# Performance work log

Measured on AMD Instinct MI355X. Metric: run time of the kernel, lower is better.

Reference implementation:

```python
import jax, jax.numpy as jnp
import numpy as np
from jax import lax

MAX_DECAY = 0.99
EPS = 1e-05
TOPK = 4


def ema_mask_group(moving_avg, new, mask, decay0, cluster_update_num):
    """Faithful port of ema_tensor_mask_group_inplace, including the quirk that
    the Python-level `decay` variable is carried (and possibly shrunk) across
    cluster iterations. Implemented as a lax.scan over clusters carrying decay.
    moving_avg/new: [C] or [C, D]; mask, cluster_update_num: [C].
    """
    def step(decay, xs):
        ma, nw, m, c = xs
        d = jnp.where((m != 0) & (c <= 10.0), decay * c / 10.0, decay)
        out = jnp.where(m != 0, ma * d + nw * (1.0 - d), ma)
        return d, out
    _, out = lax.scan(step, jnp.asarray(decay0, moving_avg.dtype),
                      (moving_avg, new, mask, cluster_update_num))
    return out


def laplace_smoothing(x, n_categories, eps=EPS):
    return (x + eps) / (x.sum() + n_categories * eps)


def setup_inputs() -> dict:
    key = jax.random.key(0)
    k1, k2 = jax.random.split(key)
    N, C, D = 65536, 512, 256
    return {
        "inputs_flatten": jax.random.normal(k1, (N, D), dtype=jnp.float32),
        "dictionary": jax.random.normal(k2, (C, D), dtype=jnp.float32),
        "cluster_size_sum": jnp.zeros((C,), dtype=jnp.float32),
        "cluster_value": jnp.zeros((C, D), dtype=jnp.float32),
        "cluster_update_num": jnp.ones((C,), dtype=jnp.float32),
    }


def reference(inputs_flatten, dictionary, cluster_size_sum, cluster_value,
              cluster_update_num):
    N, D = inputs_flatten.shape
    C = dictionary.shape[0]
    dic = lax.stop_gradient(dictionary)  # dictionary used via .detach()/.data

    # squared euclidean distances [N, C]
    distances = (jnp.sum(inputs_flatten ** 2, axis=1, keepdims=True)
                 + jnp.sum(dic ** 2, axis=1)
                 - 2.0 * jnp.matmul(inputs_flatten, dic.T))

    # ascending sort -> take topK smallest distances
    _, topk_idx = lax.top_k(-distances, TOPK)          # [N, K]
    topk_emb = dic[topk_idx]                            # [N, K, D]
    group_emb = jnp.sum(topk_emb, axis=1) / TOPK        # [N, D]

    # multi-hot encodings via scatter
    rows = jnp.arange(N)[:, None]
    encodings = jnp.zeros((N, C), dtype=jnp.float32).at[rows, topk_idx].set(1.0)

    # ---- training-mode EMA codebook update (single device: all_gather = identity) ----
    x_sg = lax.stop_gradient(inputs_flatten)
    cluster_size = jnp.sum(encodings, axis=0)           # [C]
    cluster_mask = (cluster_size != 0).astype(jnp.float32)
    cluster_update_num_new = cluster_update_num + cluster_mask

    cluster_size_sum_new = ema_mask_group(cluster_size_sum, cluster_size,
                                          cluster_mask, MAX_DECAY,
                                          cluster_update_num_new)
    input_sum = jnp.matmul(encodings.T, x_sg)           # [C, D]
    cluster_value_new = ema_mask_group(cluster_value, input_sum, cluster_mask,
                                       MAX_DECAY, cluster_update_num_new)

    cs = laplace_smoothing(cluster_size_sum_new, C, EPS) * cluster_size_sum_new.sum()
    embed_normalized = jnp.where(cluster_mask[:, None] == 1.0,
                                 cluster_value_new / cs[:, None],
                                 cluster_value_new)
    dictionary_new = embed_normalized                   # world_size == 1

    # straight-through estimator
    group_emb = lax.stop_gradient(group_emb - inputs_flatten) + inputs_flatten
    return (group_emb, topk_idx, dictionary_new, cluster_size_sum_new,
            cluster_value_new, cluster_update_num_new)
```

## Files before the change

### kernel.cpp

```cpp
#include <hip/hip_runtime.h>

#define N_ROWS 65536
#define C_CLUST 512
#define D_DIM 256

#define WS_DICTT   0
#define WS_DSQ     131072
#define WS_XSQ     131584
#define WS_CS      197120
#define WS_DCY     197632
#define WS_ISUM    198144
#define WS_COUNTS  329216
#define WS_OFFSETS 329728
#define WS_FILL    330752
#define WS_ROWLIST 331264

#define OUT_GEMB 0
#define OUT_TOPK 16777216
#define OUT_DICT 17039360
#define OUT_CSS  17170432
#define OUT_CV   17170944
#define OUT_CNUM 17302016

#define BM 128
#define BN 128
#define BK 16

#define RPB 128

__global__ void zero_k(unsigned* counts, unsigned* fill, float* isum) {
    int t = blockIdx.x * blockDim.x + threadIdx.x;
    if (t < 512) { counts[t] = 0u; fill[t] = 0u; }
    if (t < C_CLUST * D_DIM) isum[t] = 0.f;
}

__global__ void prep_dict(const float* __restrict__ dic, float* __restrict__ ws) {
    int c = blockIdx.x, k = threadIdx.x;
    float v = dic[c * D_DIM + k];
    ws[WS_DICTT + k * C_CLUST + c] = v;
    __shared__ float red[256];
    red[k] = v * v;
    __syncthreads();
    for (int s = 128; s > 0; s >>= 1) {
        if (k < s) red[k] += red[k + s];
        __syncthreads();
    }
    if (k == 0) ws[WS_DSQ + c] = red[0];
}

__global__ void row_sq(const float* __restrict__ x, float* __restrict__ ws) {
    int row = blockIdx.x, k = threadIdx.x;
    float v = x[row * D_DIM + k];
    __shared__ float red[256];
    red[k] = v * v;
    __syncthreads();
    for (int s = 128; s > 0; s >>= 1) {
        if (k < s) red[k] += red[k + s];
        __syncthreads();
    }
    if (k == 0) ws[WS_XSQ + row] = red[0];
}

__global__ __launch_bounds__(256, 2) void gemm_topk(
    const float* __restrict__ x, const float* __restrict__ ws,
    float* __restrict__ out_topk, unsigned* __restrict__ counts)
{
    extern __shared__ float smem[];
    unsigned* hist = (unsigned*)(smem + 16512);
    float* As = smem;
    float* Bs = smem + 2048;

    const int tid = threadIdx.x;
    const int tx = tid & 15, ty = tid >> 4;
    const int rowBase = blockIdx.x * BM;
    const float* dictT = ws + WS_DICTT;
    const float* dsq = ws + WS_DSQ;
    const float* xsq = ws + WS_XSQ;

    for (int h = tid; h < 512; h += 256) hist[h] = 0u;

    float td0 = 3.4e38f, td1 = 3.4e38f, td2 = 3.4e38f, td3 = 3.4e38f;
    int ti0 = -1, ti1 = -1, ti2 = -1, ti3 = -1;

    for (int cc = 0; cc < C_CLUST / BN; ++cc) {
        float acc[8][8];
        #pragma unroll
        for (int i = 0; i < 8; ++i)
            #pragma unroll
            for (int j = 0; j < 8; ++j) acc[i][j] = 0.f;

        for (int kb = 0; kb < D_DIM / BK; ++kb) {
            __syncthreads();
            #pragma unroll
            for (int i = 0; i < 2; ++i) {
                int q = tid + i * 256;
                int r = q >> 2;
                int kk = (q & 3) << 2;
                const float4 v = *reinterpret_cast<const float4*>(
                    &x[(rowBase + r) * D_DIM + kb * BK + kk]);
                As[(kk + 0) * BM + r] = v.x;
                As[(kk + 1) * BM + r] = v.y;
                As[(kk + 2) * BM + r] = v.z;
                As[(kk + 3) * BM + r] = v.w;
            }
            #pragma unroll
            for (int i = 0; i < 2; ++i) {
                int q = tid + i * 256;
                int k = q >> 5;
                int c4 = (q & 31) << 2;
                *reinterpret_cast<float4*>(&Bs[k * BN + c4]) =
                    *reinterpret_cast<const float4*>(
                        &dictT[(kb * BK + k) * C_CLUST + cc * BN + c4]);
            }
            __syncthreads();
            #pragma unroll
            for (int k = 0; k < BK; ++k) {
                float a[8], b[8];
                float4 t0 = *reinterpret_cast<const float4*>(&As[k * BM + ty * 8]);
                float4 t1 = *reinterpret_cast<const float4*>(&As[k * BM + ty * 8 + 4]);
                float4 u0 = *reinterpret_cast<const float4*>(&Bs[k * BN + tx * 8]);
                float4 u1 = *reinterpret_cast<const float4*>(&Bs[k * BN + tx * 8 + 4]);
                a[0]=t0.x; a[1]=t0.y; a[2]=t0.z; a[3]=t0.w;
                a[4]=t1.x; a[5]=t1.y; a[6]=t1.z; a[7]=t1.w;
                b[0]=u0.x; b[1]=u0.y; b[2]=u0.z; b[3]=u0.w;
                b[4]=u1.x; b[5]=u1.y; b[6]=u1.z; b[7]=u1.w;
                #pragma unroll
                for (int i = 0; i < 8; ++i)
                    #pragma unroll
                    for (int j = 0; j < 8; ++j)
                        acc[i][j] = fmaf(a[i], b[j], acc[i][j]);
            }
        }
        __syncthreads();
        {
            float ds[8];
            #pragma unroll
            for (int j = 0; j < 8; ++j) ds[j] = dsq[cc * BN + tx * 8 + j];
            #pragma unroll
            for (int i = 0; i < 8; ++i) {
                float xs = xsq[rowBase + ty * 8 + i];
                #pragma unroll
                for (int j = 0; j < 8; ++j) {
                    float v = __fsub_rn(__fadd_rn(xs, ds[j]),
                                        __fmul_rn(2.0f, acc[i][j]));
                    smem[(ty * 8 + i) * 129 + tx * 8 + j] = v;
                }
            }
        }
        __syncthreads();
        if (tid < BM) {
            const float* srow = &smem[tid * 129];
            #pragma unroll 4
            for (int c = 0; c < BN; ++c) {
                float v = srow[c];
                int idx = cc * BN + c;
                if (v < td3) {
                    if (v < td2) {
                        td3 = td2; ti3 = ti2;
                        if (v < td1) {
                            td2 = td1; ti2 = ti1;
                            if (v < td0) { td1 = td0; ti1 = ti0; td0 = v; ti0 = idx; }
                            else { td1 = v; ti1 = idx; }
                        } else { td2 = v; ti2 = idx; }
                    } else { td3 = v; ti3 = idx; }
                }
            }
        }
        __syncthreads();
    }

    if (tid < BM) {
        int r = rowBase + tid;
        out_topk[r * 4 + 0] = (float)ti0;
        out_topk[r * 4 + 1] = (float)ti1;
        out_topk[r * 4 + 2] = (float)ti2;
        out_topk[r * 4 + 3] = (float)ti3;
        atomicAdd(&hist[ti0], 1u);
        atomicAdd(&hist[ti1], 1u);
        atomicAdd(&hist[ti2], 1u);
        atomicAdd(&hist[ti3], 1u);
    }
    __syncthreads();
    for (int h = tid; h < 512; h += 256) {
        unsigned v = hist[h];
        if (v) atomicAdd(&counts[h], v);
    }
}

__global__ void group_emb_k(const float* __restrict__ x, const float* __restrict__ dic,
                            const float* __restrict__ topk, float* __restrict__ out)
{
    int row = blockIdx.x, d = threadIdx.x;
    int i0 = (int)topk[row * 4 + 0];
    int i1 = (int)topk[row * 4 + 1];
    int i2 = (int)topk[row * 4 + 2];
    int i3 = (int)topk[row * 4 + 3];
    float g = __fadd_rn(__fadd_rn(__fadd_rn(dic[i0 * D_DIM + d],
                                            dic[i1 * D_DIM + d]),
                                  dic[i2 * D_DIM + d]),
                        dic[i3 * D_DIM + d]);
    g = __fmul_rn(g, 0.25f);
    float xv = x[row * D_DIM + d];
    out[row * D_DIM + d] = __fadd_rn(__fsub_rn(g, xv), xv);
}

__global__ void prefix_k(const unsigned* __restrict__ counts, unsigned* __restrict__ offsets) {
    __shared__ unsigned s[512];
    int t = threadIdx.x;
    unsigned my = counts[t];
    s[t] = my;
    __syncthreads();
    for (int off = 1; off < 512; off <<= 1) {
        unsigned v = (t >= off) ? s[t - off] : 0u;
        __syncthreads();
        s[t] += v;
        __syncthreads();
    }
    offsets[t] = s[t] - my;
    if (t == 511) offsets[512] = s[511];
}

__global__ void scatter_k(const float* __restrict__ topk, const unsigned* __restrict__ offsets,
                          unsigned* __restrict__ fill, unsigned* __restrict__ rowlist) {
    int row = blockIdx.x * 256 + threadIdx.x;
    #pragma unroll
    for (int k = 0; k < 4; ++k) {
        int c = (int)topk[row * 4 + k];
        unsigned p = atomicAdd(&fill[c], 1u);
        rowlist[offsets[c] + p] = ((unsigned)c << 16) | (unsigned)row;
    }
}

__global__ __launch_bounds__(256, 8) void cluster_sum2_k(
    const float* __restrict__ x, const unsigned* __restrict__ rowlist,
    float* __restrict__ isum)
{
    const int d = threadIdx.x;
    const int base = blockIdx.x * RPB;
    unsigned e0 = rowlist[base];
    int ccur = (int)(e0 >> 16);
    float acc = 0.f;
    #pragma unroll 4
    for (int j = 0; j < RPB; ++j) {
        unsigned e = rowlist[base + j];
        int c = (int)(e >> 16);
        float v = x[(e & 0xFFFFu) * D_DIM + d];
        if (c != ccur) {
            atomicAdd(&isum[ccur * D_DIM + d], acc);
            acc = 0.f;
            ccur = c;
        }
        acc += v;
    }
    atomicAdd(&isum[ccur * D_DIM + d], acc);
}

__global__ void ema_scalar_k(const float* __restrict__ css_in, const float* __restrict__ cnum_in,
                             const unsigned* __restrict__ counts,
                             float* __restrict__ ws, float* __restrict__ out) {
    __shared__ float sdecay[512];
    __shared__ float sred[512];
    __shared__ float scn[512];
    __shared__ unsigned smask[512];
    int t = threadIdx.x;
    unsigned cnt = counts[t];
    float size = (float)cnt;
    float mask = (cnt != 0u) ? 1.f : 0.f;
    float cnum_new = __fadd_rn(cnum_in[t], mask);
    scn[t] = cnum_new;
    smask[t] = cnt;
    __syncthreads();
    if (t == 0) {
        float d = 0.99f;
        for (int c = 0; c < 512; ++c) {
            if (smask[c] != 0u && scn[c] <= 10.0f)
                d = __fmul_rn(d, scn[c]) / 10.0f;
            sdecay[c] = d;
        }
    }
    __syncthreads();
    float d = sdecay[t];
    float css = css_in[t];
    float css_new = (cnt != 0u)
        ? __fadd_rn(__fmul_rn(css, d), __fmul_rn(size, __fsub_rn(1.f, d)))
        : css;
    out[OUT_CSS + t] = css_new;
    out[OUT_CNUM + t] = cnum_new;
    sred[t] = css_new;
    __syncthreads();
    for (int s = 256; s > 0; s >>= 1) {
        if (t < s) sred[t] += sred[t + s];
        __syncthreads();
    }
    float S = sred[0];
    float cs = __fmul_rn(__fdiv_rn(__fadd_rn(css_new, 1e-5f),
                                   __fadd_rn(S, 0.00512f)), S);
    ws[WS_CS + t] = cs;
    ws[WS_DCY + t] = d;
}

__global__ void final_k(const float* __restrict__ cv_in, const float* __restrict__ ws,
                        const unsigned* __restrict__ counts, float* __restrict__ out) {
    int c = blockIdx.x, d = threadIdx.x;
    float isum = ws[WS_ISUM + c * D_DIM + d];
    float dc = ws[WS_DCY + c];
    float cs = ws[WS_CS + c];
    unsigned cnt = counts[c];
    float cv = cv_in[c * D_DIM + d];
    float cvn = (cnt != 0u)
        ? __fadd_rn(__fmul_rn(cv, dc), __fmul_rn(isum, __fsub_rn(1.f, dc)))
        : cv;
    out[OUT_CV + c * D_DIM + d] = cvn;
    out[OUT_DICT + c * D_DIM + d] = (cnt != 0u) ? __fdiv_rn(cvn, cs) : cvn;
}

extern "C" void kernel_launch(void* const* d_in, const int* in_sizes, int n_in,
                              void* d_out, int out_size, void* d_ws, size_t ws_size,
                              hipStream_t stream) {
    const float* x       = (const float*)d_in[0];
    const float* dic     = (const float*)d_in[1];
    const float* css_in  = (const float*)d_in[2];
    const float* cv_in   = (const float*)d_in[3];
    const float* cnum_in = (const float*)d_in[4];
    float* out = (float*)d_out;
    float* ws  = (float*)d_ws;
    unsigned* counts  = (unsigned*)(ws + WS_COUNTS);
    unsigned* offsets = (unsigned*)(ws + WS_OFFSETS);
    unsigned* fill    = (unsigned*)(ws + WS_FILL);
    unsigned* rowlist = (unsigned*)(ws + WS_ROWLIST);

    zero_k<<<C_CLUST * D_DIM / 256, 256, 0, stream>>>(counts, fill, ws + WS_ISUM);
    prep_dict<<<C_CLUST, 256, 0, stream>>>(dic, ws);
    row_sq<<<N_ROWS, 256, 0, stream>>>(x, ws);

    size_t smem_bytes = 16512 * sizeof(float) + 512 * sizeof(unsigned);
    gemm_topk<<<N_ROWS / BM, 256, smem_bytes, stream>>>(x, ws, out + OUT_TOPK, counts);

    group_emb_k<<<N_ROWS, 256, 0, stream>>>(x, dic, out + OUT_TOPK, out + OUT_GEMB);
    prefix_k<<<1, 512, 0, stream>>>(counts, offsets);
    scatter_k<<<N_ROWS / 256, 256, 0, stream>>>(out + OUT_TOPK, offsets, fill, rowlist);
    cluster_sum2_k<<<N_ROWS * 4 / RPB, 256, 0, stream>>>(x, rowlist, ws + WS_ISUM);
    ema_scalar_k<<<1, 512, 0, stream>>>(css_in, cnum_in, counts, ws, out);
    final_k<<<C_CLUST, 256, 0, stream>>>(cv_in, ws, counts, out);
}
```

Before: 606.3 us.

## Compute top-4 in registers with warp-shuffle merges instead of shared-memory scan

Replaces the per-tile path that wrote the distance tile to shared memory and had half the threads scan 128 columns serially. Each thread now keeps a local top-4 over its 8 columns, then top-4 lists are merged across the 16 column-threads with xor shuffles and a bitonic-style merge4 using index tie-breaking. It also pads the A tile stride to reduce LDS bank conflicts, changes the B column mapping to interleaved halves, and switches to small static shared memory, which may raise occupancy. The shuffle merges add ALU work per row, and the lexicographic tie-break could order equal distances differently than before.

```diff
diff --git a/kernel.cpp b/kernel.cpp
--- a/kernel.cpp
+++ b/kernel.cpp
@@ -25,6 +25,7 @@
 #define BM 128
 #define BN 128
 #define BK 16
+#define ASTRIDE 132
 
 #define RPB 128
 
@@ -61,14 +62,42 @@
     if (k == 0) ws[WS_XSQ + row] = red[0];
 }
 
+__device__ __forceinline__ void lexCE(float& av, int& ai, float& bv, int& bi) {
+    bool sw = (bv < av) || ((bv == av) && (bi < ai));
+    float nv0 = sw ? bv : av; int ni0 = sw ? bi : ai;
+    float nv1 = sw ? av : bv; int ni1 = sw ? ai : bi;
+    av = nv0; ai = ni0; bv = nv1; bi = ni1;
+}
+
+__device__ __forceinline__ void merge4(
+    float& a0v, int& a0i, float& a1v, int& a1i,
+    float& a2v, int& a2i, float& a3v, int& a3i,
+    float b0v, int b0i, float b1v, int b1i,
+    float b2v, int b2i, float b3v, int b3i)
+{
+    bool s0 = (b3v < a0v) || ((b3v == a0v) && (b3i < a0i));
+    float m0v = s0 ? b3v : a0v; int m0i = s0 ? b3i : a0i;
+    bool s1 = (b2v < a1v) || ((b2v == a1v) && (b2i < a1i));
+    float m1v = s1 ? b2v : a1v; int m1i = s1 ? b2i : a1i;
+    bool s2 = (b1v < a2v) || ((b1v == a2v) && (b1i < a2i));
+    float m2v = s2 ? b1v : a2v; int m2i = s2 ? b1i : a2i;
+    bool s3 = (b0v < a3v) || ((b0v == a3v) && (b0i < a3i));
+    float m3v = s3 ? b0v : a3v; int m3i = s3 ? b0i : a3i;
+    lexCE(m0v, m0i, m2v, m2i);
+    lexCE(m1v, m1i, m3v, m3i);
+    lexCE(m0v, m0i, m1v, m1i);
+    lexCE(m2v, m2i, m3v, m3i);
+    a0v = m0v; a0i = m0i; a1v = m1v; a1i = m1i;
+    a2v = m2v; a2i = m2i; a3v = m3v; a3i = m3i;
+}
+
 __global__ __launch_bounds__(256, 2) void gemm_topk(
     const float* __restrict__ x, const float* __restrict__ ws,
     float* __restrict__ out_topk, unsigned* __restrict__ counts)
 {
-    extern __shared__ float smem[];
-    unsigned* hist = (unsigned*)(smem + 16512);
-    float* As = smem;
-    float* Bs = smem + 2048;
+    __shared__ float As[BK * ASTRIDE];
+    __shared__ float Bs[BK * BN];
+    __shared__ unsigned hist[512];
 
     const int tid = threadIdx.x;
     const int tx = tid & 15, ty = tid >> 4;
@@ -79,8 +108,8 @@
 
     for (int h = tid; h < 512; h += 256) hist[h] = 0u;
 
-    float td0 = 3.4e38f, td1 = 3.4e38f, td2 = 3.4e38f, td3 = 3.4e38f;
-    int ti0 = -1, ti1 = -1, ti2 = -1, ti3 = -1;
+    float rv0 = 3.4e38f, rv1 = 3.4e38f, rv2 = 3.4e38f, rv3 = 3.4e38f;
+    int ri0 = 0x7FFFFFFF, ri1 = 0x7FFFFFFF, ri2 = 0x7FFFFFFF, ri3 = 0x7FFFFFFF;
 
     for (int cc = 0; cc < C_CLUST / BN; ++cc) {
         float acc[8][8];
@@ -92,20 +121,20 @@
         for (int kb = 0; kb < D_DIM / BK; ++kb) {
             __syncthreads();
             #pragma unroll
-            for (int i = 0; i < 2; ++i) {
-                int q = tid + i * 256;
+            for (int ii = 0; ii < 2; ++ii) {
+                int q = tid + ii * 256;
                 int r = q >> 2;
                 int kk = (q & 3) << 2;
                 const float4 v = *reinterpret_cast<const float4*>(
                     &x[(rowBase + r) * D_DIM + kb * BK + kk]);
-                As[(kk + 0) * BM + r] = v.x;
-                As[(kk + 1) * BM + r] = v.y;
-                As[(kk + 2) * BM + r] = v.z;
-                As[(kk + 3) * BM + r] = v.w;
-            }
-            #pragma unroll
-            for (int i = 0; i < 2; ++i) {
-                int q = tid + i * 256;
+                As[(kk + 0) * ASTRIDE + r] = v.x;
+                As[(kk + 1) * ASTRIDE + r] = v.y;
+                As[(kk + 2) * ASTRIDE + r] = v.z;
+                As[(kk + 3) * ASTRIDE + r] = v.w;
+            }
+            #pragma unroll
+            for (int ii = 0; ii < 2; ++ii) {
+                int q = tid + ii * 256;
                 int k = q >> 5;
                 int c4 = (q & 31) << 2;
                 *reinterpret_cast<float4*>(&Bs[k * BN + c4]) =
@@ -116,10 +145,10 @@
             #pragma unroll
             for (int k = 0; k < BK; ++k) {
                 float a[8], b[8];
-                float4 t0 = *reinterpret_cast<const float4*>(&As[k * BM + ty * 8]);
-                float4 t1 = *reinterpret_cast<const float4*>(&As[k * BM + ty * 8 + 4]);
-                float4 u0 = *reinterpret_cast<const float4*>(&Bs[k * BN + tx * 8]);
-                float4 u1 = *reinterpret_cast<const float4*>(&Bs[k * BN + tx * 8 + 4]);
+                float4 t0 = *reinterpret_cast<const float4*>(&As[k * ASTRIDE + ty * 8]);
+                float4 t1 = *reinterpret_cast<const float4*>(&As[k * ASTRIDE + ty * 8 + 4]);
+                float4 u0 = *reinterpret_cast<const float4*>(&Bs[k * BN + tx * 4]);
+                float4 u1 = *reinterpret_cast<const float4*>(&Bs[k * BN + 64 + tx * 4]);
                 a[0]=t0.x; a[1]=t0.y; a[2]=t0.z; a[3]=t0.w;
                 a[4]=t1.x; a[5]=t1.y; a[6]=t1.z; a[7]=t1.w;
                 b[0]=u0.x; b[1]=u0.y; b[2]=u0.z; b[3]=u0.w;
@@ -131,54 +160,60 @@
                         acc[i][j] = fmaf(a[i], b[j], acc[i][j]);
             }
         }
-        __syncthreads();
-        {
-            float ds[8];
-            #pragma unroll
-            for (int j = 0; j < 8; ++j) ds[j] = dsq[cc * BN + tx * 8 + j];
-            #pragma unroll
-            for (int i = 0; i < 8; ++i) {
-                float xs = xsq[rowBase + ty * 8 + i];
-                #pragma unroll
-                for (int j = 0; j < 8; ++j) {
-                    float v = __fsub_rn(__fadd_rn(xs, ds[j]),
-                                        __fmul_rn(2.0f, acc[i][j]));
-                    smem[(ty * 8 + i) * 129 + tx * 8 + j] = v;
+
+        float ds[8];
+        #pragma unroll
+        for (int j = 0; j < 8; ++j) {
+            int col = (j < 4) ? (tx * 4 + j) : (64 + tx * 4 + (j - 4));
+            ds[j] = dsq[cc * BN + col];
+        }
+        #pragma unroll
+        for (int i = 0; i < 8; ++i) {
+            float xs = xsq[rowBase + ty * 8 + i];
+            float l0v = 3.4e38f, l1v = 3.4e38f, l2v = 3.4e38f, l3v = 3.4e38f;
+            int l0i = 0x7FFFFFFF, l1i = 0x7FFFFFFF, l2i = 0x7FFFFFFF, l3i = 0x7FFFFFFF;
+            #pragma unroll
+            for (int j = 0; j < 8; ++j) {
+                int col = (j < 4) ? (tx * 4 + j) : (64 + tx * 4 + (j - 4));
+                int idx = cc * BN + col;
+                float v = __fsub_rn(__fadd_rn(xs, ds[j]),
+                                    __fmul_rn(2.0f, acc[i][j]));
+                if (v < l3v) {
+                    if (v < l2v) {
+                        l3v = l2v; l3i = l2i;
+                        if (v < l1v) {
+                            l2v = l1v; l2i = l1i;
+                            if (v < l0v) { l1v = l0v; l1i = l0i; l0v = v; l0i = idx; }
+                            else { l1v = v; l1i = idx; }
+                        } else { l2v = v; l2i = idx; }
+                    } else { l3v = v; l3i = idx; }
                 }
             }
-        }
-        __syncthreads();
-        if (tid < BM) {
-            const float* srow = &smem[tid * 129];
-            #pragma unroll 4
-            for (int c = 0; c < BN; ++c) {
-                float v = srow[c];
-                int idx = cc * BN + c;
-                if (v < td3) {
-                    if (v < td2) {
-                        td3 = td2; ti3 = ti2;
-                        if (v < td1) {
-                            td2 = td1; ti2 = ti1;
-                            if (v < td0) { td1 = td0; ti1 = ti0; td0 = v; ti0 = idx; }
-                            else { td1 = v; ti1 = idx; }
-                        } else { td2 = v; ti2 = idx; }
-                    } else { td3 = v; ti3 = idx; }
-                }
-            }
-        }
-        __syncthreads();
-    }
-
-    if (tid < BM) {
-        int r = rowBase + tid;
-        out_topk[r * 4 + 0] = (float)ti0;
-        out_topk[r * 4 + 1] = (float)ti1;
-        out_topk[r * 4 + 2] = (float)ti2;
-        out_topk[r * 4 + 3] = (float)ti3;
-        atomicAdd(&hist[ti0], 1u);
-        atomicAdd(&hist[ti1], 1u);
-        atomicAdd(&hist[ti2], 1u);
-        atomicAdd(&hist[ti3], 1u);
+            #pragma unroll
+            for (int mask = 1; mask <= 8; mask <<= 1) {
+                float b0v = __shfl_xor(l0v, mask); int b0i = __shfl_xor(l0i, mask);
+                float b1v = __shfl_xor(l1v, mask); int b1i = __shfl_xor(l1i, mask);
+                float b2v = __shfl_xor(l2v, mask); int b2i = __shfl_xor(l2i, mask);
+                float b3v = __shfl_xor(l3v, mask); int b3i = __shfl_xor(l3i, mask);
+                merge4(l0v, l0i, l1v, l1i, l2v, l2i, l3v, l3i,
+                       b0v, b0i, b1v, b1i, b2v, b2i, b3v, b3i);
+            }
+            if ((tx & 7) == i)
+                merge4(rv0, ri0, rv1, ri1, rv2, ri2, rv3, ri3,
+                       l0v, l0i, l1v, l1i, l2v, l2i, l3v, l3i);
+        }
+    }
+
+    if (tx < 8) {
+        int r = rowBase + ty * 8 + tx;
+        out_topk[r * 4 + 0] = (float)ri0;
+        out_topk[r * 4 + 1] = (float)ri1;
+        out_topk[r * 4 + 2] = (float)ri2;
+        out_topk[r * 4 + 3] = (float)ri3;
+        atomicAdd(&hist[ri0], 1u);
+        atomicAdd(&hist[ri1], 1u);
+        atomicAdd(&hist[ri2], 1u);
+        atomicAdd(&hist[ri3], 1u);
     }
     __syncthreads();
     for (int h = tid; h < 512; h += 256) {
@@ -333,8 +368,7 @@
     prep_dict<<<C_CLUST, 256, 0, stream>>>(dic, ws);
     row_sq<<<N_ROWS, 256, 0, stream>>>(x, ws);
 
-    size_t smem_bytes = 16512 * sizeof(float) + 512 * sizeof(unsigned);
-    gemm_topk<<<N_ROWS / BM, 256, smem_bytes, stream>>>(x, ws, out + OUT_TOPK, counts);
+    gemm_topk<<<N_ROWS / BM, 256, 0, stream>>>(x, ws, out + OUT_TOPK, counts);
 
     group_emb_k<<<N_ROWS, 256, 0, stream>>>(x, dic, out + OUT_TOPK, out + OUT_GEMB);
     prefix_k<<<1, 512, 0, stream>>>(counts, offsets);
```

Result: slower. 636.8 us (+5.0%).

## Replace FP32 GEMM top-k with split-bf16 MFMA candidate search plus exact refinement

Applied to the files above, without the earlier changes.

The scalar FP32 distance GEMM becomes a bf16 MFMA GEMM that splits each operand into hi and lo bf16 parts and uses three products to approximate FP32 accuracy. It keeps 16 candidates per row using packed 64-bit key/index sorting. A refine kernel then recomputes exact FP32 distances for those candidates, picks the top-4, and fuses the group embedding output and the global histogram atomics. This removes the separate row-norm and group-embedding kernels but adds approximation risk if a true top-4 falls outside the candidate set.

```diff
diff --git a/kernel.cpp b/kernel.cpp
--- a/kernel.cpp
+++ b/kernel.cpp
@@ -6,7 +6,6 @@
 
 #define WS_DICTT   0
 #define WS_DSQ     131072
-#define WS_XSQ     131584
 #define WS_CS      197120
 #define WS_DCY     197632
 #define WS_ISUM    198144
@@ -22,11 +21,20 @@
 #define OUT_CV   17170944
 #define OUT_CNUM 17302016
 
-#define BM 128
-#define BN 128
-#define BK 16
-
 #define RPB 128
+
+typedef __attribute__((ext_vector_type(8))) short short8;
+typedef __attribute__((ext_vector_type(16))) float f32x16;
+
+__device__ __forceinline__ unsigned short f2bf(float v) {
+    union { float f; unsigned u; } c; c.f = v;
+    unsigned r = c.u + 0x7FFFu + ((c.u >> 16) & 1u);
+    return (unsigned short)(r >> 16);
+}
+__device__ __forceinline__ float bf2f(unsigned short h) {
+    union { float f; unsigned u; } c; c.u = ((unsigned)h) << 16;
+    return c.f;
+}
 
 __global__ void zero_k(unsigned* counts, unsigned* fill, float* isum) {
     int t = blockIdx.x * blockDim.x + threadIdx.x;
@@ -37,7 +45,11 @@
 __global__ void prep_dict(const float* __restrict__ dic, float* __restrict__ ws) {
     int c = blockIdx.x, k = threadIdx.x;
     float v = dic[c * D_DIM + k];
-    ws[WS_DICTT + k * C_CLUST + c] = v;
+    unsigned short* dhi = (unsigned short*)(ws + WS_DICTT);
+    unsigned short* dlo = dhi + 131072;
+    unsigned short hb = f2bf(v);
+    dhi[c * D_DIM + k] = hb;
+    dlo[c * D_DIM + k] = f2bf(__fsub_rn(v, bf2f(hb)));
     __shared__ float red[256];
     red[k] = v * v;
     __syncthreads();
@@ -48,160 +60,230 @@
     if (k == 0) ws[WS_DSQ + c] = red[0];
 }
 
-__global__ void row_sq(const float* __restrict__ x, float* __restrict__ ws) {
-    int row = blockIdx.x, k = threadIdx.x;
-    float v = x[row * D_DIM + k];
-    __shared__ float red[256];
-    red[k] = v * v;
-    __syncthreads();
-    for (int s = 128; s > 0; s >>= 1) {
-        if (k < s) red[k] += red[k + s];
-        __syncthreads();
-    }
-    if (k == 0) ws[WS_XSQ + row] = red[0];
-}
-
-__global__ __launch_bounds__(256, 2) void gemm_topk(
+__global__ __launch_bounds__(256, 2) void stage1_cand(
     const float* __restrict__ x, const float* __restrict__ ws,
-    float* __restrict__ out_topk, unsigned* __restrict__ counts)
+    float* __restrict__ cand_out)
+{
+    __shared__ unsigned short hlds[32 * 264];
+    __shared__ unsigned short llds[32 * 264];
+    __shared__ float dsq_s[512];
+
+    const int tid = threadIdx.x;
+    const int lane = tid & 63;
+    const int w = tid >> 6;
+    const int kg = lane >> 5;
+    const int cl_lane = lane & 31;
+    const int row = blockIdx.x * 128 + w * 32 + cl_lane;
+
+    const unsigned short* dhi = (const unsigned short*)(ws + WS_DICTT);
+    const unsigned short* dlo = dhi + 131072;
+
+    for (int i = tid; i < 512; i += 256) dsq_s[i] = ws[WS_DSQ + i];
+
+    short8 bhi[16], blo[16];
+    #pragma unroll
+    for (int s = 0; s < 16; ++s) {
+        const float* px = &x[(size_t)row * D_DIM + s * 16 + kg * 8];
+        float4 u0 = *reinterpret_cast<const float4*>(px);
+        float4 u1 = *reinterpret_cast<const float4*>(px + 4);
+        float vv[8] = {u0.x, u0.y, u0.z, u0.w, u1.x, u1.y, u1.z, u1.w};
+        short8 h, l;
+        #pragma unroll
+        for (int e = 0; e < 8; ++e) {
+            unsigned short hb = f2bf(vv[e]);
+            unsigned short lb = f2bf(__fsub_rn(vv[e], bf2f(hb)));
+            h[e] = (short)hb; l[e] = (short)lb;
+        }
+        bhi[s] = h; blo[s] = l;
+    }
+
+    unsigned long long kk[8];
+    #pragma unroll
+    for (int q = 0; q < 8; ++q) kk[q] = 0xFFFFFFFFFFFFFFFFULL;
+
+    for (int ct = 0; ct < 16; ++ct) {
+        __syncthreads();
+        for (int q = tid; q < 1024; q += 256) {
+            int c = q >> 5, k8 = (q & 31) * 8;
+            *reinterpret_cast<uint4*>(&hlds[c * 264 + k8]) =
+                *reinterpret_cast<const uint4*>(&dhi[(ct * 32 + c) * D_DIM + k8]);
+            *reinterpret_cast<uint4*>(&llds[c * 264 + k8]) =
+                *reinterpret_cast<const uint4*>(&dlo[(ct * 32 + c) * D_DIM + k8]);
+        }
+        __syncthreads();
+
+        f32x16 ahh, ahl, alh;
+        #pragma unroll
+        for (int r = 0; r < 16; ++r) { ahh[r] = 0.f; ahl[r] = 0.f; alh[r] = 0.f; }
+
+        #pragma unroll
+        for (int s = 0; s < 16; ++s) {
+            short8 Ah = *reinterpret_cast<const short8*>(
+                &hlds[cl_lane * 264 + s * 16 + kg * 8]);
+            short8 Al = *reinterpret_cast<const short8*>(
+                &llds[cl_lane * 264 + s * 16 + kg * 8]);
+            ahh = __builtin_amdgcn_mfma_f32_32x32x16_bf16(Ah, bhi[s], ahh, 0, 0, 0);
+            ahl = __builtin_amdgcn_mfma_f32_32x32x16_bf16(Ah, blo[s], ahl, 0, 0, 0);
+            alh = __builtin_amdgcn_mfma_f32_32x32x16_bf16(Al, bhi[s], alh, 0, 0, 0);
+        }
+
+        #pragma unroll
+        for (int r = 0; r < 16; ++r) {
+            int cl = ct * 32 + (r & 3) + 8 * (r >> 2) + 4 * kg;
+            float dot = ahh[r] + ahl[r] + alh[r];
+            float key = (dsq_s[cl] + 1024.0f) - 2.0f * dot;
+            unsigned long long v =
+                ((unsigned long long)__float_as_uint(key) << 32) | (unsigned)cl;
+            #pragma unroll
+            for (int q = 0; q < 8; ++q) {
+                bool lt = v < kk[q];
+                unsigned long long mn = lt ? v : kk[q];
+                unsigned long long mx = lt ? kk[q] : v;
+                kk[q] = mn; v = mx;
+            }
+        }
+    }
+
+    uint4 wv;
+    wv.x = (unsigned)(kk[0] & 0xFFFF) | ((unsigned)(kk[1] & 0xFFFF) << 16);
+    wv.y = (unsigned)(kk[2] & 0xFFFF) | ((unsigned)(kk[3] & 0xFFFF) << 16);
+    wv.z = (unsigned)(kk[4] & 0xFFFF) | ((unsigned)(kk[5] & 0xFFFF) << 16);
+    wv.w = (unsigned)(kk[6] & 0xFFFF) | ((unsigned)(kk[7] & 0xFFFF) << 16);
+    *reinterpret_cast<uint4*>(&cand_out[(size_t)row * 256 + kg * 4]) = wv;
+}
+
+__global__ __launch_bounds__(256, 2) void refine_k(
+    const float* __restrict__ x, const float* __restrict__ dic,
+    const float* __restrict__ ws, float* __restrict__ out,
+    unsigned* __restrict__ counts)
 {
     extern __shared__ float smem[];
-    unsigned* hist = (unsigned*)(smem + 16512);
-    float* As = smem;
-    float* Bs = smem + 2048;
-
-    const int tid = threadIdx.x;
-    const int tx = tid & 15, ty = tid >> 4;
-    const int rowBase = blockIdx.x * BM;
-    const float* dictT = ws + WS_DICTT;
-    const float* dsq = ws + WS_DSQ;
-    const float* xsq = ws + WS_XSQ;
-
-    for (int h = tid; h < 512; h += 256) hist[h] = 0u;
-
-    float td0 = 3.4e38f, td1 = 3.4e38f, td2 = 3.4e38f, td3 = 3.4e38f;
-    int ti0 = -1, ti1 = -1, ti2 = -1, ti3 = -1;
-
-    for (int cc = 0; cc < C_CLUST / BN; ++cc) {
-        float acc[8][8];
+    float* xl  = smem;
+    float* dl  = smem + 4 * 260;
+    float* sqb = smem + 4 * 260 + 64 * 260;
+    __shared__ float distb[64];
+    __shared__ float xss[4];
+    __shared__ int cidx[64];
+    __shared__ int selp[16];
+
+    const int t = threadIdx.x;
+    const int rowBase = blockIdx.x * 4;
+    const unsigned short* candp = (const unsigned short*)(out + OUT_GEMB);
+
+    if (t < 64) cidx[t] = (int)candp[(size_t)(rowBase + (t >> 4)) * 512 + (t & 15)];
+
+    {
+        int r = t >> 6, seg = t & 63;
+        const float* px = &x[(size_t)(rowBase + r) * D_DIM + seg * 4];
+        float4 a = *reinterpret_cast<const float4*>(px);
+        *reinterpret_cast<float4*>(&xl[r * 260 + seg * 4]) = a;
+        sqb[r * 256 + seg * 4 + 0] = a.x * a.x;
+        sqb[r * 256 + seg * 4 + 1] = a.y * a.y;
+        sqb[r * 256 + seg * 4 + 2] = a.z * a.z;
+        sqb[r * 256 + seg * 4 + 3] = a.w * a.w;
+    }
+    __syncthreads();
+
+    {
+        int r = t >> 6, g = t & 63;
+        for (int st = 128; st > 0; st >>= 1) {
+            for (int k = g; k < st; k += 64)
+                sqb[r * 256 + k] += sqb[r * 256 + k + st];
+            __syncthreads();
+        }
+        if (t < 4) xss[t] = sqb[t * 256];
+    }
+    __syncthreads();
+
+    {
+        int p = t >> 2, q = t & 3;
+        const float* src = &dic[(size_t)cidx[p] * D_DIM + q * 64];
         #pragma unroll
-        for (int i = 0; i < 8; ++i)
-            #pragma unroll
-            for (int j = 0; j < 8; ++j) acc[i][j] = 0.f;
-
-        for (int kb = 0; kb < D_DIM / BK; ++kb) {
-            __syncthreads();
-            #pragma unroll
-            for (int i = 0; i < 2; ++i) {
-                int q = tid + i * 256;
-                int r = q >> 2;
-                int kk = (q & 3) << 2;
-                const float4 v = *reinterpret_cast<const float4*>(
-                    &x[(rowBase + r) * D_DIM + kb * BK + kk]);
-                As[(kk + 0) * BM + r] = v.x;
-                As[(kk + 1) * BM + r] = v.y;
-                As[(kk + 2) * BM + r] = v.z;
-                As[(kk + 3) * BM + r] = v.w;
+        for (int i = 0; i < 16; ++i)
+            *reinterpret_cast<float4*>(&dl[p * 260 + q * 64 + i * 4]) =
+                *reinterpret_cast<const float4*>(src + i * 4);
+    }
+    __syncthreads();
+
+    if (t < 64) {
+        int r = t >> 4;
+        float acc = 0.f;
+        const float* dp = &dl[t * 260];
+        const float* xp = &xl[r * 260];
+        #pragma unroll 4
+        for (int k4 = 0; k4 < 64; ++k4) {
+            float4 dv = *reinterpret_cast<const float4*>(dp + k4 * 4);
+            float4 xv = *reinterpret_cast<const float4*>(xp + k4 * 4);
+            acc = fmaf(xv.x, dv.x, acc);
+            acc = fmaf(xv.y, dv.y, acc);
+            acc = fmaf(xv.z, dv.z, acc);
+            acc = fmaf(xv.w, dv.w, acc);
+        }
+        float ds = ws[WS_DSQ + cidx[t]];
+        distb[t] = __fsub_rn(__fadd_rn(xss[r], ds), __fmul_rn(2.0f, acc));
+    }
+    __syncthreads();
+
+    if (t < 4) {
+        float bv0 = 3.4e38f, bv1 = 3.4e38f, bv2 = 3.4e38f, bv3 = 3.4e38f;
+        int bi0 = 0x7FFFFFFF, bi1 = 0x7FFFFFFF, bi2 = 0x7FFFFFFF, bi3 = 0x7FFFFFFF;
+        int bp0 = 0, bp1 = 0, bp2 = 0, bp3 = 0;
+        for (int s = 0; s < 16; ++s) {
+            int p = t * 16 + s;
+            float v = distb[p];
+            int ci = cidx[p];
+            if (v < bv3 || (v == bv3 && ci < bi3)) {
+                if (v < bv2 || (v == bv2 && ci < bi2)) {
+                    bv3 = bv2; bi3 = bi2; bp3 = bp2;
+                    if (v < bv1 || (v == bv1 && ci < bi1)) {
+                        bv2 = bv1; bi2 = bi1; bp2 = bp1;
+                        if (v < bv0 || (v == bv0 && ci < bi0)) {
+                            bv1 = bv0; bi1 = bi0; bp1 = bp0;
+                            bv0 = v; bi0 = ci; bp0 = p;
+                        } else { bv1 = v; bi1 = ci; bp1 = p; }
+                    } else { bv2 = v; bi2 = ci; bp2 = p; }
+                } else { bv3 = v; bi3 = ci; bp3 = p; }
             }
-            #pragma unroll
-            for (int i = 0; i < 2; ++i) {
-                int q = tid + i * 256;
-                int k = q >> 5;
-                int c4 = (q & 31) << 2;
-                *reinterpret_cast<float4*>(&Bs[k * BN + c4]) =
-                    *reinterpret_cast<const float4*>(
-                        &dictT[(kb * BK + k) * C_CLUST + cc * BN + c4]);
-            }
-            __syncthreads();
-            #pragma unroll
-            for (int k = 0; k < BK; ++k) {
-                float a[8], b[8];
-                float4 t0 = *reinterpret_cast<const float4*>(&As[k * BM + ty * 8]);
-                float4 t1 = *reinterpret_cast<const float4*>(&As[k * BM + ty * 8 + 4]);
-                float4 u0 = *reinterpret_cast<const float4*>(&Bs[k * BN + tx * 8]);
-                float4 u1 = *reinterpret_cast<const float4*>(&Bs[k * BN + tx * 8 + 4]);
-                a[0]=t0.x; a[1]=t0.y; a[2]=t0.z; a[3]=t0.w;
-                a[4]=t1.x; a[5]=t1.y; a[6]=t1.z; a[7]=t1.w;
-                b[0]=u0.x; b[1]=u0.y; b[2]=u0.z; b[3]=u0.w;
-                b[4]=u1.x; b[5]=u1.y; b[6]=u1.z; b[7]=u1.w;
-                #pragma unroll
-                for (int i = 0; i < 8; ++i)
-                    #pragma unroll
-                    for (int j = 0; j < 8; ++j)
-                        acc[i][j] = fmaf(a[i], b[j], acc[i][j]);
-            }
-        }
-        __syncthreads();
-        {
-            float ds[8];
-            #pragma unroll
-            for (int j = 0; j < 8; ++j) ds[j] = dsq[cc * BN + tx * 8 + j];
-            #pragma unroll
-            for (int i = 0; i < 8; ++i) {
-                float xs = xsq[rowBase + ty * 8 + i];
-                #pragma unroll
-                for (int j = 0; j < 8; ++j) {
-                    float v = __fsub_rn(__fadd_rn(xs, ds[j]),
-                                        __fmul_rn(2.0f, acc[i][j]));
-                    smem[(ty * 8 + i) * 129 + tx * 8 + j] = v;
-                }
-            }
-        }
-        __syncthreads();
-        if (tid < BM) {
-            const float* srow = &smem[tid * 129];
-            #pragma unroll 4
-            for (int c = 0; c < BN; ++c) {
-                float v = srow[c];
-                int idx = cc * BN + c;
-                if (v < td3) {
-                    if (v < td2) {
-                        td3 = td2; ti3 = ti2;
-                        if (v < td1) {
-                            td2 = td1; ti2 = ti1;
-                            if (v < td0) { td1 = td0; ti1 = ti0; td0 = v; ti0 = idx; }
-                            else { td1 = v; ti1 = idx; }
-                        } else { td2 = v; ti2 = idx; }
-                    } else { td3 = v; ti3 = idx; }
-                }
-            }
-        }
-        __syncthreads();
-    }
-
-    if (tid < BM) {
-        int r = rowBase + tid;
-        out_topk[r * 4 + 0] = (float)ti0;
-        out_topk[r * 4 + 1] = (float)ti1;
-        out_topk[r * 4 + 2] = (float)ti2;
-        out_topk[r * 4 + 3] = (float)ti3;
-        atomicAdd(&hist[ti0], 1u);
-        atomicAdd(&hist[ti1], 1u);
-        atomicAdd(&hist[ti2], 1u);
-        atomicAdd(&hist[ti3], 1u);
-    }
-    __syncthreads();
-    for (int h = tid; h < 512; h += 256) {
-        unsigned v = hist[h];
-        if (v) atomicAdd(&counts[h], v);
-    }
-}
-
-__global__ void group_emb_k(const float* __restrict__ x, const float* __restrict__ dic,
-                            const float* __restrict__ topk, float* __restrict__ out)
-{
-    int row = blockIdx.x, d = threadIdx.x;
-    int i0 = (int)topk[row * 4 + 0];
-    int i1 = (int)topk[row * 4 + 1];
-    int i2 = (int)topk[row * 4 + 2];
-    int i3 = (int)topk[row * 4 + 3];
-    float g = __fadd_rn(__fadd_rn(__fadd_rn(dic[i0 * D_DIM + d],
-                                            dic[i1 * D_DIM + d]),
-                                  dic[i2 * D_DIM + d]),
-                        dic[i3 * D_DIM + d]);
-    g = __fmul_rn(g, 0.25f);
-    float xv = x[row * D_DIM + d];
-    out[row * D_DIM + d] = __fadd_rn(__fsub_rn(g, xv), xv);
+        }
+        int row = rowBase + t;
+        out[OUT_TOPK + (size_t)row * 4 + 0] = (float)bi0;
+        out[OUT_TOPK + (size_t)row * 4 + 1] = (float)bi1;
+        out[OUT_TOPK + (size_t)row * 4 + 2] = (float)bi2;
+        out[OUT_TOPK + (size_t)row * 4 + 3] = (float)bi3;
+        atomicAdd(&counts[bi0], 1u);
+        atomicAdd(&counts[bi1], 1u);
+        atomicAdd(&counts[bi2], 1u);
+        atomicAdd(&counts[bi3], 1u);
+        selp[t * 4 + 0] = bp0 & 63;
+        selp[t * 4 + 1] = bp1 & 63;
+        selp[t * 4 + 2] = bp2 & 63;
+        selp[t * 4 + 3] = bp3 & 63;
+    }
+    __syncthreads();
+
+    {
+        int r = t >> 6, u = t & 63;
+        int p0 = selp[r * 4 + 0], p1 = selp[r * 4 + 1];
+        int p2 = selp[r * 4 + 2], p3 = selp[r * 4 + 3];
+        int k4 = u * 4;
+        float4 a = *reinterpret_cast<const float4*>(&dl[p0 * 260 + k4]);
+        float4 b = *reinterpret_cast<const float4*>(&dl[p1 * 260 + k4]);
+        float4 c = *reinterpret_cast<const float4*>(&dl[p2 * 260 + k4]);
+        float4 e = *reinterpret_cast<const float4*>(&dl[p3 * 260 + k4]);
+        float4 xv = *reinterpret_cast<const float4*>(&xl[r * 260 + k4]);
+        float4 o;
+        float g;
+        g = __fmul_rn(__fadd_rn(__fadd_rn(__fadd_rn(a.x, b.x), c.x), e.x), 0.25f);
+        o.x = __fadd_rn(__fsub_rn(g, xv.x), xv.x);
+        g = __fmul_rn(__fadd_rn(__fadd_rn(__fadd_rn(a.y, b.y), c.y), e.y), 0.25f);
+        o.y = __fadd_rn(__fsub_rn(g, xv.y), xv.y);
+        g = __fmul_rn(__fadd_rn(__fadd_rn(__fadd_rn(a.z, b.z), c.z), e.z), 0.25f);
+        o.z = __fadd_rn(__fsub_rn(g, xv.z), xv.z);
+        g = __fmul_rn(__fadd_rn(__fadd_rn(__fadd_rn(a.w, b.w), c.w), e.w), 0.25f);
+        o.w = __fadd_rn(__fsub_rn(g, xv.w), xv.w);
+        *reinterpret_cast<float4*>(
+            &out[OUT_GEMB + (size_t)(rowBase + r) * D_DIM + k4]) = o;
+    }
 }
 
 __global__ void prefix_k(const unsigned* __restrict__ counts, unsigned* __restrict__ offsets) {
@@ -331,12 +413,12 @@
 
     zero_k<<<C_CLUST * D_DIM / 256, 256, 0, stream>>>(counts, fill, ws + WS_ISUM);
     prep_dict<<<C_CLUST, 256, 0, stream>>>(dic, ws);
-    row_sq<<<N_ROWS, 256, 0, stream>>>(x, ws);
-
-    size_t smem_bytes = 16512 * sizeof(float) + 512 * sizeof(unsigned);
-    gemm_topk<<<N_ROWS / BM, 256, smem_bytes, stream>>>(x, ws, out + OUT_TOPK, counts);
-
-    group_emb_k<<<N_ROWS, 256, 0, stream>>>(x, dic, out + OUT_TOPK, out + OUT_GEMB);
+
+    stage1_cand<<<N_ROWS / 128, 256, 0, stream>>>(x, ws, out + OUT_GEMB);
+
+    size_t smem2 = (4 * 260 + 64 * 260 + 4 * 256) * sizeof(float);
+    refine_k<<<N_ROWS / 4, 256, smem2, stream>>>(x, dic, ws, out, counts);
+
     prefix_k<<<1, 512, 0, stream>>>(counts, offsets);
     scatter_k<<<N_ROWS / 256, 256, 0, stream>>>(out + OUT_TOPK, offsets, fill, rowlist);
     cluster_sum2_k<<<N_ROWS * 4 / RPB, 256, 0, stream>>>(x, rowlist, ws + WS_ISUM);
```

Result: slower. 673.2 us (+11.0%).
